# Performance work log

Hardware: AMD Instinct MI355X
Metric: run time of the kernel (lower is better)

Reference implementation:

```python
import jax, jax.numpy as jnp
import numpy as np

B, N, QD, D, S, H, K = 4, 1024, 320, 512, 1024, 8, 32
DH = D // H  # 64
EPS = 1e-5


def setup_inputs() -> dict:
    key = jax.random.key(0)
    ks = jax.random.split(key, 10)
    sc = 1.0 / np.sqrt(D)
    return {
        "query_states": jax.random.normal(ks[0], (B, N, QD), dtype=jnp.float32),
        "Wqp": jax.random.normal(ks[1], (D, QD), dtype=jnp.float32) / np.sqrt(QD),
        "mem_keys": jax.random.normal(ks[2], (S, D), dtype=jnp.float32),
        "mem_values": jax.random.normal(ks[3], (S, D), dtype=jnp.float32) * 0.1,
        "Wq": jax.random.normal(ks[4], (D, D), dtype=jnp.float32) * sc,
        "Wk": jax.random.normal(ks[5], (D, D), dtype=jnp.float32) * sc,
        "Wv": jax.random.normal(ks[6], (D, D), dtype=jnp.float32) * sc,
        "Wo": jax.random.normal(ks[7], (D, D), dtype=jnp.float32) * sc,
        "ln_g": jnp.ones((D,), dtype=jnp.float32),
        "ln_b": jnp.zeros((D,), dtype=jnp.float32),
        "Wout": jax.random.normal(ks[8], (QD, D), dtype=jnp.float32) * sc,
        "bout": jnp.zeros((QD,), dtype=jnp.float32),
    }


def _l2norm(x):
    return x / jnp.sqrt(jnp.sum(x * x, axis=-1, keepdims=True) + 1e-12)


def reference(query_states, Wqp, mem_keys, mem_values, Wq, Wk, Wv, Wo, ln_g, ln_b, Wout, bout):
    # project queries into memory space: [B,N,D]
    q = jnp.einsum("bnq,dq->bnd", query_states, Wqp)
    # normalize memory slots (normalize_slots=True)
    keys = _l2norm(mem_keys)    # [S,D]
    vals = _l2norm(mem_values)  # [S,D]
    # top-k memory-slot preselection over raw query-key scores
    scores = jnp.einsum("bnd,sd->bns", q, keys)          # [B,N,S]
    _, top_idx = jax.lax.top_k(scores, K)                  # [B,N,K]
    sel_k = jnp.take(keys, top_idx, axis=0)                # [B,N,K,D]
    sel_v = jnp.take(vals, top_idx, axis=0)                # [B,N,K,D]
    # multi-head cross-attention over gathered slots
    qh = jnp.einsum("bnd,ed->bne", q, Wq).reshape(B, N, H, DH)
    kh = jnp.einsum("bnkd,ed->bnke", sel_k, Wk).reshape(B, N, K, H, DH)
    vh = jnp.einsum("bnkd,ed->bnke", sel_v, Wv).reshape(B, N, K, H, DH)
    att = jnp.einsum("bnhd,bnkhd->bnhk", qh, kh) / jnp.sqrt(jnp.float32(DH))  # temperature=1.0
    w = jax.nn.softmax(att, axis=-1)                       # [B,N,H,K]
    ctx = jnp.einsum("bnhk,bnkhd->bnhd", w, vh).reshape(B, N, D)
    ctx = jnp.einsum("bnd,ed->bne", ctx, Wo)               # [B,N,D]
    # output projector: LayerNorm + Linear(memory_dim -> query_dim); dropout inactive (eval)
    mu = jnp.mean(ctx, axis=-1, keepdims=True)
    var = jnp.mean((ctx - mu) ** 2, axis=-1, keepdims=True)
    normed = (ctx - mu) / jnp.sqrt(var + EPS) * ln_g + ln_b
    out = jnp.einsum("bnd,qd->bnq", normed, Wout) + bout   # [B,N,QD]
    return out
```

## Files before the change

kernel.cpp:

```cpp
#include <hip/hip_runtime.h>


__device__ __forceinline__ float bf2f(unsigned short u) {
    return __uint_as_float(((unsigned int)u) << 16);
}
__device__ __forceinline__ unsigned short f2bf(float f) {
    unsigned int u = __float_as_uint(f);
    u += 0x7FFFu + ((u >> 16) & 1u);
    return (unsigned short)(u >> 16);
}
__device__ __forceinline__ int detect_bf(const void* g) {
    return ((*(const unsigned int*)g) & 0xFFFFu) != 0u;
}
__device__ __forceinline__ float ldg1(const void* p, size_t i, int bf) {
    return bf ? bf2f(((const unsigned short*)p)[i]) : ((const float*)p)[i];
}
__device__ __forceinline__ void ld4(const void* p, size_t i, int bf, float* o) {
    if (bf) {
        ushort4 v = *reinterpret_cast<const ushort4*>((const unsigned short*)p + i);
        o[0] = bf2f(v.x); o[1] = bf2f(v.y); o[2] = bf2f(v.z); o[3] = bf2f(v.w);
    } else {
        float4 v = *reinterpret_cast<const float4*>((const float*)p + i);
        o[0] = v.x; o[1] = v.y; o[2] = v.z; o[3] = v.w;
    }
}
__device__ __forceinline__ unsigned int fkey(float x) {
    unsigned int u = __float_as_uint(x);
    return (u & 0x80000000u) ? ~u : (u | 0x80000000u);
}
__device__ __forceinline__ float funkey(unsigned int k) {
    unsigned int u = (k & 0x80000000u) ? (k & 0x7FFFFFFFu) : ~k;
    return __uint_as_float(u);
}

typedef __attribute__((ext_vector_type(8))) short bf16x8;
typedef __attribute__((ext_vector_type(4))) float f32x4;
typedef __attribute__((ext_vector_type(4))) unsigned int u32x4;

__device__ __forceinline__ void split8(const float* x, u32x4& h, u32x4& l) {
#pragma unroll
    for (int j = 0; j < 4; j++) {
        float x0 = x[2 * j], x1 = x[2 * j + 1];
        unsigned int hp, lp;
        asm("v_cvt_pk_bf16_f32 %0, %1, %2" : "=v"(hp) : "v"(x0), "v"(x1));
        float h0 = __uint_as_float(hp << 16);
        float h1 = __uint_as_float(hp & 0xFFFF0000u);
        float l0 = x0 - h0, l1 = x1 - h1;
        asm("v_cvt_pk_bf16_f32 %0, %1, %2" : "=v"(lp) : "v"(l0), "v"(l1));
        h[j] = hp; l[j] = lp;
    }
}

__device__ __forceinline__ void gload16(const void* g, void* l) {
    __builtin_amdgcn_global_load_lds(
        (const __attribute__((address_space(1))) unsigned int*)g,
        (__attribute__((address_space(3))) unsigned int*)l,
        16, 0, 0);
}

__global__ __launch_bounds__(256) void prep_fused(
    const void* __restrict__ keys, const void* __restrict__ vals,
    const void* __restrict__ Wqp, const void* __restrict__ X,
    const void* __restrict__ gdet,
    float* __restrict__ inv_kf, float* __restrict__ inv_vf,
    float* __restrict__ WqpT,
    unsigned short* __restrict__ Xh, unsigned short* __restrict__ Xl)
{
    __shared__ double red[256];
    __shared__ float tile[32][36];
    const int bf = detect_bf(gdet);
    const int bid = blockIdx.x, t = threadIdx.x;
    if (bid < 2048) {
        int r = bid;
        const void* src = (r < 1024) ? keys : vals;
        size_t base = (size_t)((r < 1024) ? r : r - 1024) * 512;
        float x0 = ldg1(src, base + t, bf), x1 = ldg1(src, base + t + 256, bf);
        red[t] = (double)x0 * x0 + (double)x1 * x1;
        __syncthreads();
        for (int s = 128; s > 0; s >>= 1) {
            if (t < s) red[t] += red[t + s];
            __syncthreads();
        }
        if (t == 0) {
            float rs = (float)(1.0 / sqrt(red[0] + 1e-12));
            if (r < 1024) inv_kf[r] = rs;
            else          inv_vf[r - 1024] = rs;
        }
    } else if (bid < 2208) {
        int tid = bid - 2048;
        int d0 = (tid & 15) * 32, q0 = (tid >> 4) * 32;
        int r = t >> 3, c = (t & 7) * 4;
        float v[4];
        ld4(Wqp, (size_t)(d0 + r) * 320 + q0 + c, bf, v);
#pragma unroll
        for (int i = 0; i < 4; i++) tile[r][c + i] = v[i];
        __syncthreads();
        float o[4];
#pragma unroll
        for (int i = 0; i < 4; i++) o[i] = tile[c + i][r];
        *reinterpret_cast<float4*>(&WqpT[(size_t)(q0 + r) * 512 + d0 + c]) =
            make_float4(o[0], o[1], o[2], o[3]);
    } else {
        int i = (bid - 2208) * 256 + t;
        float v[8];
        ld4(X, (size_t)i * 8, bf, v);
        ld4(X, (size_t)i * 8 + 4, bf, v + 4);
        u32x4 h, l;
        split8(v, h, l);
        *reinterpret_cast<u32x4*>(Xh + (size_t)i * 8) = h;
        *reinterpret_cast<u32x4*>(Xl + (size_t)i * 8) = l;
    }
}

__global__ __launch_bounds__(256) void mfma_abt(
    const void* __restrict__ A, const void* __restrict__ B,
    const float* __restrict__ scale, float* __restrict__ C,
    const void* __restrict__ A2, const void* __restrict__ B2,
    const float* __restrict__ scale2, float* __restrict__ C2, int ysplit,
    const float2* __restrict__ stats, const void* __restrict__ g,
    const void* __restrict__ bvec, const void* __restrict__ bias,
    void* __restrict__ O,
    unsigned short* __restrict__ Hout, unsigned short* __restrict__ Lout,
    int hrow0a, int hrow0b,
    int N, int amode, int abfon, int bbfon, int epi, int npass,
    const void* __restrict__ gdet)
{
    __shared__ __align__(16) short lds[12288];
    const int AHo = 0, ALo = 2048, BHo = 4096, BLo = 8192;
    const int flag = detect_bf(gdet);
    const int abf = abfon ? flag : 0;
    const int bbf = bbfon ? flag : 0;
    const int t = threadIdx.x;
    int by = blockIdx.y;
    const void* Ap = A; const void* Bp = B;
    const float* scp = scale; float* Cp = C;
    int hrow0 = hrow0a;
    if (ysplit && by >= ysplit) {
        Ap = A2; Bp = B2; scp = scale2; Cp = C2; by -= ysplit; hrow0 = hrow0b;
    }
    const int m0 = by * 32, n0 = blockIdx.x * 64;
    const int lane = t & 63, wv = t >> 6;
    const int wm = wv >> 1, wn = wv & 1;
    const int srow = t >> 3;
    const int sc8  = t & 7;

    int aoff[2], boff[2][2];
#pragma unroll
    for (int kk = 0; kk < 2; kk++) {
        int ra = wm * 16 + (lane & 15);
        int ca = kk * 4 + (lane >> 4);
        aoff[kk] = ra * 64 + ((ca ^ (ra & 7)) << 3);
    }
#pragma unroll
    for (int ni = 0; ni < 2; ni++)
#pragma unroll
        for (int kk = 0; kk < 2; kk++) {
            int rb = wn * 32 + ni * 16 + (lane & 15);
            int cb = kk * 4 + (lane >> 4);
            boff[ni][kk] = rb * 64 + ((cb ^ (rb & 7)) << 3);
        }

    const int addr0 = srow * 64 + ((sc8 ^ (srow & 7)) << 3);
    const int addr1 = addr0 + 32 * 64;

    float s0 = 1.0f;
    float2 st0 = make_float2(0.f, 1.f);
    if (amode == 1) {
        s0 = scp ? scp[m0 + srow] : 1.0f;
    } else if (amode == 2) {
        st0 = stats[m0 + srow];
    }

    f32x4 acc[2];
    acc[0] = (f32x4){0.f, 0.f, 0.f, 0.f};
    acc[1] = (f32x4){0.f, 0.f, 0.f, 0.f};

    float av0[8], bv0[8], bv1[8];
    {
        ld4(Ap, (size_t)(m0 + srow) * 512 + sc8 * 8,          abf, av0);
        ld4(Ap, (size_t)(m0 + srow) * 512 + sc8 * 8 + 4,      abf, av0 + 4);
        ld4(Bp, (size_t)(n0 + srow) * 512 + sc8 * 8,          bbf, bv0);
        ld4(Bp, (size_t)(n0 + srow) * 512 + sc8 * 8 + 4,      bbf, bv0 + 4);
        ld4(Bp, (size_t)(n0 + srow + 32) * 512 + sc8 * 8,     bbf, bv1);
        ld4(Bp, (size_t)(n0 + srow + 32) * 512 + sc8 * 8 + 4, bbf, bv1 + 4);
    }

    for (int ks = 0; ks < 8; ks++) {
        const int kb = ks * 64;
        float a0[8], b0[8], b1[8];
#pragma unroll
        for (int j = 0; j < 8; j++) { a0[j] = av0[j]; b0[j] = bv0[j]; b1[j] = bv1[j]; }
        if (amode == 1) {
#pragma unroll
            for (int j = 0; j < 8; j++) a0[j] *= s0;
        } else if (amode == 2) {
            float gv[8], bv8[8];
            ld4(g,    (size_t)(kb + sc8 * 8),     flag, gv);
            ld4(g,    (size_t)(kb + sc8 * 8 + 4), flag, gv + 4);
            ld4(bvec, (size_t)(kb + sc8 * 8),     flag, bv8);
            ld4(bvec, (size_t)(kb + sc8 * 8 + 4), flag, bv8 + 4);
#pragma unroll
            for (int j = 0; j < 8; j++)
                a0[j] = (a0[j] - st0.x) * st0.y * gv[j] + bv8[j];
        }
        u32x4 ah0, al0, bh0, bl0, bh1, bl1;
        split8(a0, ah0, al0);
        split8(b0, bh0, bl0); split8(b1, bh1, bl1);
        __syncthreads();
        *reinterpret_cast<u32x4*>(&lds[AHo + addr0]) = ah0;
        *reinterpret_cast<u32x4*>(&lds[ALo + addr0]) = al0;
        *reinterpret_cast<u32x4*>(&lds[BHo + addr0]) = bh0;
        *reinterpret_cast<u32x4*>(&lds[BHo + addr1]) = bh1;
        *reinterpret_cast<u32x4*>(&lds[BLo + addr0]) = bl0;
        *reinterpret_cast<u32x4*>(&lds[BLo + addr1]) = bl1;
        __syncthreads();
        if (ks < 7) {
            const int kn = kb + 64;
            ld4(Ap, (size_t)(m0 + srow) * 512 + kn + sc8 * 8,          abf, av0);
            ld4(Ap, (size_t)(m0 + srow) * 512 + kn + sc8 * 8 + 4,      abf, av0 + 4);
            ld4(Bp, (size_t)(n0 + srow) * 512 + kn + sc8 * 8,          bbf, bv0);
            ld4(Bp, (size_t)(n0 + srow) * 512 + kn + sc8 * 8 + 4,      bbf, bv0 + 4);
            ld4(Bp, (size_t)(n0 + srow + 32) * 512 + kn + sc8 * 8,     bbf, bv1);
            ld4(Bp, (size_t)(n0 + srow + 32) * 512 + kn + sc8 * 8 + 4, bbf, bv1 + 4);
        }
        for (int p = 0; p < npass; p++) {
            const int Ab = (p == 1 || p == 3) ? ALo : AHo;
            const int Bb = (p >= 2) ? BLo : BHo;
#pragma unroll
            for (int kk = 0; kk < 2; kk++) {
                bf16x8 af, bfr[2];
                af = *reinterpret_cast<const bf16x8*>(&lds[Ab + aoff[kk]]);
#pragma unroll
                for (int ni = 0; ni < 2; ni++)
                    bfr[ni] = *reinterpret_cast<const bf16x8*>(&lds[Bb + boff[ni][kk]]);
#pragma unroll
                for (int ni = 0; ni < 2; ni++)
                    acc[ni] = __builtin_amdgcn_mfma_f32_16x16x32_bf16(
                        af, bfr[ni], acc[ni], 0, 0, 0);
            }
        }
    }

    {
        int mbase = m0 + wm * 16 + (lane >> 4) * 4;
#pragma unroll
        for (int ni = 0; ni < 2; ni++) {
            int n = n0 + wn * 32 + ni * 16 + (lane & 15);
            if (epi == 0) {
#pragma unroll
                for (int r = 0; r < 4; r++) {
                    float v = acc[ni][r];
                    Cp[(size_t)(mbase + r) * N + n] = v;
                    if (Hout) {
                        unsigned short hb = f2bf(v);
                        unsigned short lb = f2bf(v - bf2f(hb));
                        size_t ho = (size_t)(hrow0 + mbase + r) * N + n;
                        Hout[ho] = hb;
                        Lout[ho] = lb;
                    }
                }
            } else {
                float bo = bias ? ldg1(bias, n, flag) : 0.f;
#pragma unroll
                for (int r = 0; r < 4; r++) {
                    float v = acc[ni][r] + bo;
                    size_t off = (size_t)(mbase + r) * N + n;
                    if (flag) ((unsigned short*)O)[off] = f2bf(v);
                    else      ((float*)O)[off] = v;
                }
            }
        }
    }
}

__global__ __launch_bounds__(256) void gemm_scqh(
    const unsigned short* __restrict__ Xh, const unsigned short* __restrict__ Xl,
    const unsigned short* __restrict__ Bh, const unsigned short* __restrict__ Bl,
    float* __restrict__ Sc, float* __restrict__ qh)
{
    __shared__ __align__(16) short lds[24576];
    const int AHo = 0, ALo = 8192, BHo = 16384, BLo = 20480;
    const int t = threadIdx.x;
    const int m0 = blockIdx.y * 128, n0 = blockIdx.x * 64;
    const int lane = t & 63, wv = t >> 6;
    const int wm = wv >> 1, wn = wv & 1;
    const int lr = lane >> 3;
    const int lc = lane & 7;

    int aoff[4][2], boff[2][2];
#pragma unroll
    for (int mi = 0; mi < 4; mi++)
#pragma unroll
        for (int kk = 0; kk < 2; kk++) {
            int ra = wm * 64 + mi * 16 + (lane & 15);
            int ca = kk * 4 + (lane >> 4);
            aoff[mi][kk] = ra * 64 + ((ca ^ (ra & 7)) << 3);
        }
#pragma unroll
    for (int ni = 0; ni < 2; ni++)
#pragma unroll
        for (int kk = 0; kk < 2; kk++) {
            int rb = wn * 32 + ni * 16 + (lane & 15);
            int cb = kk * 4 + (lane >> 4);
            boff[ni][kk] = rb * 64 + ((cb ^ (rb & 7)) << 3);
        }

    f32x4 acc[4][2];
#pragma unroll
    for (int mi = 0; mi < 4; mi++)
#pragma unroll
        for (int ni = 0; ni < 2; ni++)
            acc[mi][ni] = (f32x4){0.f, 0.f, 0.f, 0.f};

    char* smem = (char*)lds;

    for (int ks = 0; ks < 5; ks++) {
        const int kb = ks * 64;
        __syncthreads();
#pragma unroll
        for (int i = 0; i < 4; i++) {
            int r0 = wv * 32 + i * 8;
            int r  = r0 + lr;
            int sc = lc ^ (r & 7);
            size_t go = (size_t)(m0 + r) * 320 + kb + sc * 8;
            gload16(Xh + go, smem + (AHo << 1) + r0 * 128);
            gload16(Xl + go, smem + (ALo << 1) + r0 * 128);
        }
#pragma unroll
        for (int i = 0; i < 2; i++) {
            int r0 = wv * 16 + i * 8;
            int r  = r0 + lr;
            int sc = lc ^ (r & 7);
            size_t go = (size_t)(n0 + r) * 320 + kb + sc * 8;
            gload16(Bh + go, smem + (BHo << 1) + r0 * 128);
            gload16(Bl + go, smem + (BLo << 1) + r0 * 128);
        }
        __syncthreads();
#pragma unroll
        for (int p = 0; p < 3; p++) {
            const int Ab = (p == 1) ? ALo : AHo;
            const int Bb = (p == 2) ? BLo : BHo;
#pragma unroll
            for (int kk = 0; kk < 2; kk++) {
                bf16x8 af[4], bfr[2];
#pragma unroll
                for (int mi = 0; mi < 4; mi++)
                    af[mi] = *reinterpret_cast<const bf16x8*>(&lds[Ab + aoff[mi][kk]]);
#pragma unroll
                for (int ni = 0; ni < 2; ni++)
                    bfr[ni] = *reinterpret_cast<const bf16x8*>(&lds[Bb + boff[ni][kk]]);
#pragma unroll
                for (int mi = 0; mi < 4; mi++)
#pragma unroll
                    for (int ni = 0; ni < 2; ni++)
                        acc[mi][ni] = __builtin_amdgcn_mfma_f32_16x16x32_bf16(
                            af[mi], bfr[ni], acc[mi][ni], 0, 0, 0);
            }
        }
    }

#pragma unroll
    for (int mi = 0; mi < 4; mi++) {
        int mbase = m0 + wm * 64 + mi * 16 + (lane >> 4) * 4;
#pragma unroll
        for (int ni = 0; ni < 2; ni++) {
            int n = n0 + wn * 32 + ni * 16 + (lane & 15);
#pragma unroll
            for (int r = 0; r < 4; r++) {
                float v = acc[mi][ni][r];
                int m = mbase + r;
                if (n0 < 1024) Sc[(size_t)m * 1024 + n] = v;
                else           qh[(size_t)m * 512 + (n - 1024)] = v;
            }
        }
    }
}

__global__ __launch_bounds__(256) void topk_select(
    const float* __restrict__ Sc, const void* __restrict__ X,
    const void* __restrict__ gdet, const float* __restrict__ KWf,
    int* __restrict__ idx)
{
    __shared__ unsigned int srow[4][1024];
    __shared__ unsigned int scv[4][64];
    __shared__ int          sci[4][64];
    const int bf = detect_bf(gdet);
    const int w = threadIdx.x >> 6, lane = threadIdx.x & 63;
    const int row = blockIdx.x * 4 + w;
    const float* S = Sc + (size_t)row * 1024;

#pragma unroll
    for (int q = 0; q < 4; q++) {
        float4 v = *reinterpret_cast<const float4*>(&S[lane * 4 + q * 256]);
        uint4 k = make_uint4(fkey(v.x), fkey(v.y), fkey(v.z), fkey(v.w));
        *reinterpret_cast<uint4*>(&srow[w][lane * 4 + q * 256]) = k;
    }
    scv[w][lane] = 0u;
    sci[w][lane] = 0x7FFFFFFF;
    __syncthreads();

    unsigned int lo = 0u, hi = 0xFFFFFFFFu;
    int cnt_lo = 1024;
    while (cnt_lo > 48 && hi - lo > 1u) {
        unsigned int mid = lo + ((hi - lo) >> 1);
        int c = 0;
#pragma unroll
        for (int q = 0; q < 4; q++) {
            uint4 k = *reinterpret_cast<const uint4*>(&srow[w][lane * 4 + q * 256]);
            c += (k.x >= mid) + (k.y >= mid) + (k.z >= mid) + (k.w >= mid);
        }
#pragma unroll
        for (int o = 1; o < 64; o <<= 1) c += __shfl_xor(c, o, 64);
        if (c >= 33) { lo = mid; cnt_lo = c; }
        else hi = mid;
    }
    const unsigned int T = lo;

    int cl = 0;
#pragma unroll
    for (int q = 0; q < 4; q++) {
        uint4 k = *reinterpret_cast<const uint4*>(&srow[w][lane * 4 + q * 256]);
        cl += (k.x >= T) + (k.y >= T) + (k.z >= T) + (k.w >= T);
    }
    int inc = cl;
#pragma unroll
    for (int o = 1; o < 64; o <<= 1) {
        int y = __shfl_up(inc, o, 64);
        if (lane >= o) inc += y;
    }
    int pos = inc - cl;
#pragma unroll
    for (int q = 0; q < 4; q++) {
        uint4 k = *reinterpret_cast<const uint4*>(&srow[w][lane * 4 + q * 256]);
        int base = lane * 4 + q * 256;
        if (k.x >= T && pos < 64) { scv[w][pos] = k.x; sci[w][pos] = base + 0; pos++; }
        if (k.y >= T && pos < 64) { scv[w][pos] = k.y; sci[w][pos] = base + 1; pos++; }
        if (k.z >= T && pos < 64) { scv[w][pos] = k.z; sci[w][pos] = base + 2; pos++; }
        if (k.w >= T && pos < 64) { scv[w][pos] = k.w; sci[w][pos] = base + 3; pos++; }
    }
    __syncthreads();
    unsigned int cv = scv[w][lane];
    int          ci = sci[w][lane];
#pragma unroll
    for (int k = 2; k <= 64; k <<= 1) {
#pragma unroll
        for (int jj = k >> 1; jj > 0; jj >>= 1) {
            unsigned int ov = __shfl_xor(cv, jj, 64);
            int          oi = __shfl_xor(ci, jj, 64);
            bool up = ((lane & k) == 0);
            bool takemax = (((lane & jj) == 0) == up);
            bool othergreater = (ov > cv) || (ov == cv && oi < ci);
            if (takemax == othergreater) { cv = ov; ci = oi; }
        }
    }
    float v31 = funkey(__shfl(cv, 31, 64));
    float v32 = funkey(__shfl(cv, 32, 64));
    if (v31 - v32 > 2.5e-4f) {
        if (lane < 32) idx[(size_t)row * 32 + lane] = ci;
        return;
    }
    size_t xb = (size_t)row * 320;
    bool active = (lane < 48) && (ci != 0x7FFFFFFF);
    int cidx = active ? ci : 0x7FFFFFFF;
    const float* kr = KWf + (size_t)(active ? ci : 0) * 320;
    double s = 0.0;
#pragma unroll 4
    for (int d = 0; d < 320; d++) {
        float xd = ldg1(X, xb + d, bf);
        s += (double)xd * (double)kr[d];
    }
    if (!active) s = -1.0e300;
#pragma unroll
    for (int k = 2; k <= 64; k <<= 1) {
#pragma unroll
        for (int jj = k >> 1; jj > 0; jj >>= 1) {
            double os = __shfl_xor(s, jj, 64);
            int    oi = __shfl_xor(cidx, jj, 64);
            bool up = ((lane & k) == 0);
            bool takemax = (((lane & jj) == 0) == up);
            bool og = (os > s) || (os == s && oi < cidx);
            if (takemax == og) { s = os; cidx = oi; }
        }
    }
    if (lane < 32) idx[(size_t)row * 32 + lane] = cidx;
}

__global__ __launch_bounds__(256) void attn_kernel(
    const float* __restrict__ qh, const float* __restrict__ Kp,
    const float* __restrict__ Vp, const int* __restrict__ idx,
    float* __restrict__ ctx)
{
    __shared__ float sq[512];
    __shared__ int   sidx[32];
    __shared__ float sl[8][32];
    __shared__ float sw[8][32];
    int row = blockIdx.x, t = threadIdx.x;
    int w = t >> 6, l = t & 63;
    if (t < 128)
        *reinterpret_cast<float4*>(&sq[t * 4]) =
            *reinterpret_cast<const float4*>(&qh[(size_t)row * 512 + t * 4]);
    if (t < 32) {
        int v = idx[(size_t)row * 32 + t];
        sidx[t] = (v < 0) ? 0 : (v > 1023 ? 1023 : v);
    }
    __syncthreads();

    float4 q0 = *reinterpret_cast<const float4*>(&sq[l * 8]);
    float4 q1 = *reinterpret_cast<const float4*>(&sq[l * 8 + 4]);
    int h = l >> 3;
#pragma unroll
    for (int i = 0; i < 8; i++) {
        int s = w * 8 + i;
        const float* kp = Kp + (size_t)sidx[s] * 512 + l * 8;
        float4 k0 = *reinterpret_cast<const float4*>(kp);
        float4 k1 = *reinterpret_cast<const float4*>(kp + 4);
        float p = q0.x * k0.x + q0.y * k0.y + q0.z * k0.z + q0.w * k0.w
                + q1.x * k1.x + q1.y * k1.y + q1.z * k1.z + q1.w * k1.w;
        p += __shfl_xor(p, 1, 64);
        p += __shfl_xor(p, 2, 64);
        p += __shfl_xor(p, 4, 64);
        if ((l & 7) == 0) sl[h][s] = p * 0.125f;
    }
    __syncthreads();

    int hh = t >> 5, kk = t & 31;
    float logit = sl[hh][kk];
    float m = -1e30f;
#pragma unroll
    for (int i = 0; i < 32; i++) m = fmaxf(m, sl[hh][i]);
    float ssum = 0.f;
#pragma unroll
    for (int i = 0; i < 32; i++) ssum += __expf(sl[hh][i] - m);
    sw[hh][kk] = __expf(logit - m) / ssum;
    __syncthreads();

    int c = t * 2, hc = c >> 6;
    float ax = 0.f, ay = 0.f;
#pragma unroll
    for (int k2 = 0; k2 < 32; k2++) {
        float2 vv = *reinterpret_cast<const float2*>(&Vp[(size_t)sidx[k2] * 512 + c]);
        float wgt = sw[hc][k2];
        ax += wgt * vv.x; ay += wgt * vv.y;
    }
    *reinterpret_cast<float2*>(&ctx[(size_t)row * 512 + c]) = make_float2(ax, ay);
}

__global__ __launch_bounds__(256) void ln_stats(
    const float* __restrict__ co, float2* __restrict__ stats)
{
    int w = threadIdx.x >> 6, lane = threadIdx.x & 63;
    int row = blockIdx.x * 4 + w;
    const float* p = co + (size_t)row * 512;
    float4 a = *reinterpret_cast<const float4*>(&p[lane * 8]);
    float4 b = *reinterpret_cast<const float4*>(&p[lane * 8 + 4]);
    double s  = (double)a.x + (double)a.y + (double)a.z + (double)a.w
              + (double)b.x + (double)b.y + (double)b.z + (double)b.w;
    double ss = (double)a.x * a.x + (double)a.y * a.y + (double)a.z * a.z
              + (double)a.w * a.w + (double)b.x * b.x + (double)b.y * b.y
              + (double)b.z * b.z + (double)b.w * b.w;
#pragma unroll
    for (int o = 1; o < 64; o <<= 1) {
        s  += __shfl_xor(s, o, 64);
        ss += __shfl_xor(ss, o, 64);
    }
    if (lane == 0) {
        double mu = s / 512.0, var = ss / 512.0 - mu * mu;
        stats[row] = make_float2((float)mu, (float)(1.0 / sqrt(var + 1e-5)));
    }
}

extern "C" void kernel_launch(void* const* d_in, const int* in_sizes, int n_in,
                              void* d_out, int out_size, void* d_ws, size_t ws_size,
                              hipStream_t stream)
{
    const void* X    = d_in[0];
    const void* Wqp  = d_in[1];
    const void* keys = d_in[2];
    const void* vals = d_in[3];
    const void* Wq   = d_in[4];
    const void* Wk   = d_in[5];
    const void* Wv   = d_in[6];
    const void* Wo   = d_in[7];
    const void* ln_g = d_in[8];
    const void* ln_b = d_in[9];
    const void* Wout = d_in[10];
    const void* bout = d_in[11];

    float* ws = (float*)d_ws;
    float*  Sc     = ws;
    float*  co     = ws;
    float*  Yreg   = ws + 2097152;
    float*  qh     = ws + 4194304;
    float*  Mf     = ws + 6291456;
    float*  Kp     = ws + 6291456;
    float*  KWf    = ws + 6815744;
    float*  Vp     = ws + 6815744;
    float*  WqpT   = ws + 7340032;
    int*    idx    = (int*)(ws + 7995392);
    float*  inv_kf = ws + 8128512;
    float*  inv_vf = ws + 8129536;
    unsigned short* Xh  = (unsigned short*)(ws + 8388608);
    unsigned short* Xl  = (unsigned short*)(ws + 9043968);
    unsigned short* Bh  = (unsigned short*)(ws + 9699328);
    unsigned short* Bl  = (unsigned short*)(ws + 9945088);
    float*  ctx    = Yreg;
    float2* stats  = (float2*)Yreg;

    prep_fused<<<2848, 256, 0, stream>>>(
        keys, vals, Wqp, X, ln_g, inv_kf, inv_vf, WqpT, Xh, Xl);
    mfma_abt<<<dim3(5, 48), 256, 0, stream>>>(
        keys, WqpT, inv_kf, KWf, Wq, WqpT, nullptr, Mf, 32,
        nullptr, nullptr, nullptr, nullptr, nullptr,
        Bh, Bl, 0, 1024,
        320, 1, 1, 0, 0, 4, ln_g);
    gemm_scqh<<<dim3(24, 32), 256, 0, stream>>>(Xh, Xl, Bh, Bl, Sc, qh);
    topk_select<<<1024, 256, 0, stream>>>(Sc, X, ln_g, KWf, idx);
    mfma_abt<<<dim3(8, 64), 256, 0, stream>>>(
        keys, Wk, inv_kf, Kp, vals, Wv, inv_vf, Vp, 32,
        nullptr, nullptr, nullptr, nullptr, nullptr,
        nullptr, nullptr, 0, 0,
        512, 1, 1, 1, 0, 3, ln_g);
    attn_kernel<<<4096, 256, 0, stream>>>(qh, Kp, Vp, idx, ctx);
    mfma_abt<<<dim3(8, 128), 256, 0, stream>>>(
        ctx, Wo, nullptr, co, nullptr, nullptr, nullptr, nullptr, 0,
        nullptr, nullptr, nullptr, nullptr, nullptr,
        nullptr, nullptr, 0, 0,
        512, 0, 0, 1, 0, 3, ln_g);
    ln_stats<<<1024, 256, 0, stream>>>(co, stats);
    mfma_abt<<<dim3(5, 128), 256, 0, stream>>>(
        co, Wout, nullptr, nullptr, nullptr, nullptr, nullptr, nullptr, 0,
        stats, ln_g, ln_b, bout, d_out,
        nullptr, nullptr, 0, 0,
        320, 2, 0, 1, 1, 3, ln_g);
}
```

Baseline: 227.6 us.

## Merge K/V projection into score GEMM, fuse LN stats, narrow top-k search

Merges the K/V slot projection GEMM into the score/qh GEMM launch as extra blocks, so the two run concurrently in one grid and one launch is saved. Removes the separate ln_stats kernel by having the output GEMM compute per-row mean and inverse std inline. Also seeds the top-k radix binary search with the row min/max to cut iterations. The trade-offs are redundant re-reading of each co row per column block and heterogeneous blocks within one grid. Vp moves to a new workspace offset because it would otherwise overlap KWf while top-k is still reading it.

```diff
diff --git a/kernel.cpp b/kernel.cpp
--- a/kernel.cpp
+++ b/kernel.cpp
@@ -168,7 +168,26 @@
     if (amode == 1) {
         s0 = scp ? scp[m0 + srow] : 1.0f;
     } else if (amode == 2) {
-        st0 = stats[m0 + srow];
+        if (stats) {
+            st0 = stats[m0 + srow];
+        } else {
+            double s = 0.0, ss = 0.0;
+            for (int kb2 = 0; kb2 < 512; kb2 += 64) {
+                float v8[8];
+                ld4(Ap, (size_t)(m0 + srow) * 512 + kb2 + sc8 * 8,     abf, v8);
+                ld4(Ap, (size_t)(m0 + srow) * 512 + kb2 + sc8 * 8 + 4, abf, v8 + 4);
+#pragma unroll
+                for (int j = 0; j < 8; j++) {
+                    s  += (double)v8[j];
+                    ss += (double)v8[j] * v8[j];
+                }
+            }
+            s  += __shfl_xor(s, 1, 64);  ss += __shfl_xor(ss, 1, 64);
+            s  += __shfl_xor(s, 2, 64);  ss += __shfl_xor(ss, 2, 64);
+            s  += __shfl_xor(s, 4, 64);  ss += __shfl_xor(ss, 4, 64);
+            double mu = s / 512.0, var = ss / 512.0 - mu * mu;
+            st0 = make_float2((float)mu, (float)(1.0 / sqrt(var + 1e-5)));
+        }
     }
 
     f32x4 acc[2];
@@ -273,105 +292,208 @@
     }
 }
 
-__global__ __launch_bounds__(256) void gemm_scqh(
+__global__ __launch_bounds__(256) void gemm_scqh_kv(
     const unsigned short* __restrict__ Xh, const unsigned short* __restrict__ Xl,
     const unsigned short* __restrict__ Bh, const unsigned short* __restrict__ Bl,
-    float* __restrict__ Sc, float* __restrict__ qh)
+    float* __restrict__ Sc, float* __restrict__ qh,
+    const void* __restrict__ keys, const void* __restrict__ Wk,
+    const float* __restrict__ inv_kf, float* __restrict__ Kp,
+    const void* __restrict__ vals, const void* __restrict__ Wv,
+    const float* __restrict__ inv_vf, float* __restrict__ Vp,
+    const void* __restrict__ gdet)
 {
     __shared__ __align__(16) short lds[24576];
-    const int AHo = 0, ALo = 8192, BHo = 16384, BLo = 20480;
     const int t = threadIdx.x;
-    const int m0 = blockIdx.y * 128, n0 = blockIdx.x * 64;
+    const int bid = blockIdx.x;
     const int lane = t & 63, wv = t >> 6;
     const int wm = wv >> 1, wn = wv & 1;
-    const int lr = lane >> 3;
-    const int lc = lane & 7;
-
-    int aoff[4][2], boff[2][2];
-#pragma unroll
-    for (int mi = 0; mi < 4; mi++)
+
+    if (bid < 768) {
+        const int AHo = 0, ALo = 8192, BHo = 16384, BLo = 20480;
+        const int m0 = (bid / 24) * 128, n0 = (bid % 24) * 64;
+        const int lr = lane >> 3, lc = lane & 7;
+
+        int aoff[4][2], boff[2][2];
+#pragma unroll
+        for (int mi = 0; mi < 4; mi++)
+#pragma unroll
+            for (int kk = 0; kk < 2; kk++) {
+                int ra = wm * 64 + mi * 16 + (lane & 15);
+                int ca = kk * 4 + (lane >> 4);
+                aoff[mi][kk] = ra * 64 + ((ca ^ (ra & 7)) << 3);
+            }
+#pragma unroll
+        for (int ni = 0; ni < 2; ni++)
+#pragma unroll
+            for (int kk = 0; kk < 2; kk++) {
+                int rb = wn * 32 + ni * 16 + (lane & 15);
+                int cb = kk * 4 + (lane >> 4);
+                boff[ni][kk] = rb * 64 + ((cb ^ (rb & 7)) << 3);
+            }
+
+        f32x4 acc[4][2];
+#pragma unroll
+        for (int mi = 0; mi < 4; mi++)
+#pragma unroll
+            for (int ni = 0; ni < 2; ni++)
+                acc[mi][ni] = (f32x4){0.f, 0.f, 0.f, 0.f};
+
+        char* smem = (char*)lds;
+
+        for (int ks = 0; ks < 5; ks++) {
+            const int kb = ks * 64;
+            __syncthreads();
+#pragma unroll
+            for (int i = 0; i < 4; i++) {
+                int r0 = wv * 32 + i * 8;
+                int r  = r0 + lr;
+                int sc = lc ^ (r & 7);
+                size_t go = (size_t)(m0 + r) * 320 + kb + sc * 8;
+                gload16(Xh + go, smem + (AHo << 1) + r0 * 128);
+                gload16(Xl + go, smem + (ALo << 1) + r0 * 128);
+            }
+#pragma unroll
+            for (int i = 0; i < 2; i++) {
+                int r0 = wv * 16 + i * 8;
+                int r  = r0 + lr;
+                int sc = lc ^ (r & 7);
+                size_t go = (size_t)(n0 + r) * 320 + kb + sc * 8;
+                gload16(Bh + go, smem + (BHo << 1) + r0 * 128);
+                gload16(Bl + go, smem + (BLo << 1) + r0 * 128);
+            }
+            __syncthreads();
+#pragma unroll
+            for (int p = 0; p < 3; p++) {
+                const int Ab = (p == 1) ? ALo : AHo;
+                const int Bb = (p == 2) ? BLo : BHo;
+#pragma unroll
+                for (int kk = 0; kk < 2; kk++) {
+                    bf16x8 af[4], bfr[2];
+#pragma unroll
+                    for (int mi = 0; mi < 4; mi++)
+                        af[mi] = *reinterpret_cast<const bf16x8*>(&lds[Ab + aoff[mi][kk]]);
+#pragma unroll
+                    for (int ni = 0; ni < 2; ni++)
+                        bfr[ni] = *reinterpret_cast<const bf16x8*>(&lds[Bb + boff[ni][kk]]);
+#pragma unroll
+                    for (int mi = 0; mi < 4; mi++)
+#pragma unroll
+                        for (int ni = 0; ni < 2; ni++)
+                            acc[mi][ni] = __builtin_amdgcn_mfma_f32_16x16x32_bf16(
+                                af[mi], bfr[ni], acc[mi][ni], 0, 0, 0);
+                }
+            }
+        }
+
+#pragma unroll
+        for (int mi = 0; mi < 4; mi++) {
+            int mbase = m0 + wm * 64 + mi * 16 + (lane >> 4) * 4;
+#pragma unroll
+            for (int ni = 0; ni < 2; ni++) {
+                int n = n0 + wn * 32 + ni * 16 + (lane & 15);
+#pragma unroll
+                for (int r = 0; r < 4; r++) {
+                    float v = acc[mi][ni][r];
+                    int m = mbase + r;
+                    if (n0 < 1024) Sc[(size_t)m * 1024 + n] = v;
+                    else           qh[(size_t)m * 512 + (n - 1024)] = v;
+                }
+            }
+        }
+    } else {
+        const int AHk = 0, ALk = 2048, BHk = 4096, BLk = 8192;
+        int kb_ = bid - 768;
+        int x = kb_ & 7, y = kb_ >> 3;
+        const int flag = detect_bf(gdet);
+        const void* Ap; const void* Bp; const float* scp; float* Cp;
+        if (y < 32) { Ap = keys; Bp = Wk; scp = inv_kf; Cp = Kp; }
+        else        { Ap = vals; Bp = Wv; scp = inv_vf; Cp = Vp; y -= 32; }
+        const int m0 = y * 32, n0 = x * 64;
+        const int srow = t >> 3, sc8 = t & 7;
+
+        int aoff[2], boff[2][2];
 #pragma unroll
         for (int kk = 0; kk < 2; kk++) {
-            int ra = wm * 64 + mi * 16 + (lane & 15);
+            int ra = wm * 16 + (lane & 15);
             int ca = kk * 4 + (lane >> 4);
-            aoff[mi][kk] = ra * 64 + ((ca ^ (ra & 7)) << 3);
-        }
-#pragma unroll
-    for (int ni = 0; ni < 2; ni++)
-#pragma unroll
-        for (int kk = 0; kk < 2; kk++) {
-            int rb = wn * 32 + ni * 16 + (lane & 15);
-            int cb = kk * 4 + (lane >> 4);
-            boff[ni][kk] = rb * 64 + ((cb ^ (rb & 7)) << 3);
-        }
-
-    f32x4 acc[4][2];
-#pragma unroll
-    for (int mi = 0; mi < 4; mi++)
+            aoff[kk] = ra * 64 + ((ca ^ (ra & 7)) << 3);
+        }
 #pragma unroll
         for (int ni = 0; ni < 2; ni++)
-            acc[mi][ni] = (f32x4){0.f, 0.f, 0.f, 0.f};
-
-    char* smem = (char*)lds;
-
-    for (int ks = 0; ks < 5; ks++) {
-        const int kb = ks * 64;
-        __syncthreads();
-#pragma unroll
-        for (int i = 0; i < 4; i++) {
-            int r0 = wv * 32 + i * 8;
-            int r  = r0 + lr;
-            int sc = lc ^ (r & 7);
-            size_t go = (size_t)(m0 + r) * 320 + kb + sc * 8;
-            gload16(Xh + go, smem + (AHo << 1) + r0 * 128);
-            gload16(Xl + go, smem + (ALo << 1) + r0 * 128);
-        }
-#pragma unroll
-        for (int i = 0; i < 2; i++) {
-            int r0 = wv * 16 + i * 8;
-            int r  = r0 + lr;
-            int sc = lc ^ (r & 7);
-            size_t go = (size_t)(n0 + r) * 320 + kb + sc * 8;
-            gload16(Bh + go, smem + (BHo << 1) + r0 * 128);
-            gload16(Bl + go, smem + (BLo << 1) + r0 * 128);
-        }
-        __syncthreads();
-#pragma unroll
-        for (int p = 0; p < 3; p++) {
-            const int Ab = (p == 1) ? ALo : AHo;
-            const int Bb = (p == 2) ? BLo : BHo;
 #pragma unroll
             for (int kk = 0; kk < 2; kk++) {
-                bf16x8 af[4], bfr[2];
-#pragma unroll
-                for (int mi = 0; mi < 4; mi++)
-                    af[mi] = *reinterpret_cast<const bf16x8*>(&lds[Ab + aoff[mi][kk]]);
-#pragma unroll
-                for (int ni = 0; ni < 2; ni++)
-                    bfr[ni] = *reinterpret_cast<const bf16x8*>(&lds[Bb + boff[ni][kk]]);
-#pragma unroll
-                for (int mi = 0; mi < 4; mi++)
+                int rb = wn * 32 + ni * 16 + (lane & 15);
+                int cb = kk * 4 + (lane >> 4);
+                boff[ni][kk] = rb * 64 + ((cb ^ (rb & 7)) << 3);
+            }
+
+        const int addr0 = srow * 64 + ((sc8 ^ (srow & 7)) << 3);
+        const int addr1 = addr0 + 32 * 64;
+        const float s0 = scp[m0 + srow];
+
+        f32x4 acc[2];
+        acc[0] = (f32x4){0.f, 0.f, 0.f, 0.f};
+        acc[1] = (f32x4){0.f, 0.f, 0.f, 0.f};
+
+        float av0[8], bv0[8], bv1[8];
+        ld4(Ap, (size_t)(m0 + srow) * 512 + sc8 * 8,          flag, av0);
+        ld4(Ap, (size_t)(m0 + srow) * 512 + sc8 * 8 + 4,      flag, av0 + 4);
+        ld4(Bp, (size_t)(n0 + srow) * 512 + sc8 * 8,          flag, bv0);
+        ld4(Bp, (size_t)(n0 + srow) * 512 + sc8 * 8 + 4,      flag, bv0 + 4);
+        ld4(Bp, (size_t)(n0 + srow + 32) * 512 + sc8 * 8,     flag, bv1);
+        ld4(Bp, (size_t)(n0 + srow + 32) * 512 + sc8 * 8 + 4, flag, bv1 + 4);
+
+        for (int ks = 0; ks < 8; ks++) {
+            const int kb = ks * 64;
+            float a0[8], b0[8], b1[8];
+#pragma unroll
+            for (int j = 0; j < 8; j++) { a0[j] = av0[j] * s0; b0[j] = bv0[j]; b1[j] = bv1[j]; }
+            u32x4 ah0, al0, bh0, bl0, bh1, bl1;
+            split8(a0, ah0, al0);
+            split8(b0, bh0, bl0); split8(b1, bh1, bl1);
+            __syncthreads();
+            *reinterpret_cast<u32x4*>(&lds[AHk + addr0]) = ah0;
+            *reinterpret_cast<u32x4*>(&lds[ALk + addr0]) = al0;
+            *reinterpret_cast<u32x4*>(&lds[BHk + addr0]) = bh0;
+            *reinterpret_cast<u32x4*>(&lds[BHk + addr1]) = bh1;
+            *reinterpret_cast<u32x4*>(&lds[BLk + addr0]) = bl0;
+            *reinterpret_cast<u32x4*>(&lds[BLk + addr1]) = bl1;
+            __syncthreads();
+            if (ks < 7) {
+                const int kn = kb + 64;
+                ld4(Ap, (size_t)(m0 + srow) * 512 + kn + sc8 * 8,          flag, av0);
+                ld4(Ap, (size_t)(m0 + srow) * 512 + kn + sc8 * 8 + 4,      flag, av0 + 4);
+                ld4(Bp, (size_t)(n0 + srow) * 512 + kn + sc8 * 8,          flag, bv0);
+                ld4(Bp, (size_t)(n0 + srow) * 512 + kn + sc8 * 8 + 4,      flag, bv0 + 4);
+                ld4(Bp, (size_t)(n0 + srow + 32) * 512 + kn + sc8 * 8,     flag, bv1);
+                ld4(Bp, (size_t)(n0 + srow + 32) * 512 + kn + sc8 * 8 + 4, flag, bv1 + 4);
+            }
+#pragma unroll
+            for (int p = 0; p < 3; p++) {
+                const int Ab = (p == 1) ? ALk : AHk;
+                const int Bb = (p == 2) ? BLk : BHk;
+#pragma unroll
+                for (int kk = 0; kk < 2; kk++) {
+                    bf16x8 af, bfr[2];
+                    af = *reinterpret_cast<const bf16x8*>(&lds[Ab + aoff[kk]]);
 #pragma unroll
                     for (int ni = 0; ni < 2; ni++)
-                        acc[mi][ni] = __builtin_amdgcn_mfma_f32_16x16x32_bf16(
-                            af[mi], bfr[ni], acc[mi][ni], 0, 0, 0);
-            }
-        }
-    }
-
-#pragma unroll
-    for (int mi = 0; mi < 4; mi++) {
-        int mbase = m0 + wm * 64 + mi * 16 + (lane >> 4) * 4;
+                        bfr[ni] = *reinterpret_cast<const bf16x8*>(&lds[Bb + boff[ni][kk]]);
+#pragma unroll
+                    for (int ni = 0; ni < 2; ni++)
+                        acc[ni] = __builtin_amdgcn_mfma_f32_16x16x32_bf16(
+                            af, bfr[ni], acc[ni], 0, 0, 0);
+                }
+            }
+        }
+
+        int mbase = m0 + wm * 16 + (lane >> 4) * 4;
 #pragma unroll
         for (int ni = 0; ni < 2; ni++) {
             int n = n0 + wn * 32 + ni * 16 + (lane & 15);
 #pragma unroll
-            for (int r = 0; r < 4; r++) {
-                float v = acc[mi][ni][r];
-                int m = mbase + r;
-                if (n0 < 1024) Sc[(size_t)m * 1024 + n] = v;
-                else           qh[(size_t)m * 512 + (n - 1024)] = v;
-            }
+            for (int r = 0; r < 4; r++)
+                Cp[(size_t)(mbase + r) * 512 + n] = acc[ni][r];
         }
     }
 }
@@ -389,17 +511,26 @@
     const int row = blockIdx.x * 4 + w;
     const float* S = Sc + (size_t)row * 1024;
 
+    unsigned int mn = 0xFFFFFFFFu, mx = 0u;
 #pragma unroll
     for (int q = 0; q < 4; q++) {
         float4 v = *reinterpret_cast<const float4*>(&S[lane * 4 + q * 256]);
         uint4 k = make_uint4(fkey(v.x), fkey(v.y), fkey(v.z), fkey(v.w));
         *reinterpret_cast<uint4*>(&srow[w][lane * 4 + q * 256]) = k;
+        mn = min(mn, min(min(k.x, k.y), min(k.z, k.w)));
+        mx = max(mx, max(max(k.x, k.y), max(k.z, k.w)));
     }
     scv[w][lane] = 0u;
     sci[w][lane] = 0x7FFFFFFF;
+#pragma unroll
+    for (int o = 1; o < 64; o <<= 1) {
+        mn = min(mn, __shfl_xor(mn, o, 64));
+        mx = max(mx, __shfl_xor(mx, o, 64));
+    }
     __syncthreads();
 
-    unsigned int lo = 0u, hi = 0xFFFFFFFFu;
+    unsigned int lo = mn;
+    unsigned int hi = (mx == 0xFFFFFFFFu) ? 0xFFFFFFFFu : mx + 1u;
     int cnt_lo = 1024;
     while (cnt_lo > 48 && hi - lo > 1u) {
         unsigned int mid = lo + ((hi - lo) >> 1);
@@ -545,30 +676,6 @@
     *reinterpret_cast<float2*>(&ctx[(size_t)row * 512 + c]) = make_float2(ax, ay);
 }
 
-__global__ __launch_bounds__(256) void ln_stats(
-    const float* __restrict__ co, float2* __restrict__ stats)
-{
-    int w = threadIdx.x >> 6, lane = threadIdx.x & 63;
-    int row = blockIdx.x * 4 + w;
-    const float* p = co + (size_t)row * 512;
-    float4 a = *reinterpret_cast<const float4*>(&p[lane * 8]);
-    float4 b = *reinterpret_cast<const float4*>(&p[lane * 8 + 4]);
-    double s  = (double)a.x + (double)a.y + (double)a.z + (double)a.w
-              + (double)b.x + (double)b.y + (double)b.z + (double)b.w;
-    double ss = (double)a.x * a.x + (double)a.y * a.y + (double)a.z * a.z
-              + (double)a.w * a.w + (double)b.x * b.x + (double)b.y * b.y
-              + (double)b.z * b.z + (double)b.w * b.w;
-#pragma unroll
-    for (int o = 1; o < 64; o <<= 1) {
-        s  += __shfl_xor(s, o, 64);
-        ss += __shfl_xor(ss, o, 64);
-    }
-    if (lane == 0) {
-        double mu = s / 512.0, var = ss / 512.0 - mu * mu;
-        stats[row] = make_float2((float)mu, (float)(1.0 / sqrt(var + 1e-5)));
-    }
-}
-
 extern "C" void kernel_launch(void* const* d_in, const int* in_sizes, int n_in,
                               void* d_out, int out_size, void* d_ws, size_t ws_size,
                               hipStream_t stream)
@@ -594,7 +701,6 @@
     float*  Mf     = ws + 6291456;
     float*  Kp     = ws + 6291456;
     float*  KWf    = ws + 6815744;
-    float*  Vp     = ws + 6815744;
     float*  WqpT   = ws + 7340032;
     int*    idx    = (int*)(ws + 7995392);
     float*  inv_kf = ws + 8128512;
@@ -603,8 +709,8 @@
     unsigned short* Xl  = (unsigned short*)(ws + 9043968);
     unsigned short* Bh  = (unsigned short*)(ws + 9699328);
     unsigned short* Bl  = (unsigned short*)(ws + 9945088);
+    float*  Vp     = ws + 10190848;
     float*  ctx    = Yreg;
-    float2* stats  = (float2*)Yreg;
 
     prep_fused<<<2848, 256, 0, stream>>>(
         keys, vals, Wqp, X, ln_g, inv_kf, inv_vf, WqpT, Xh, Xl);
@@ -613,23 +719,19 @@
         nullptr, nullptr, nullptr, nullptr, nullptr,
         Bh, Bl, 0, 1024,
         320, 1, 1, 0, 0, 4, ln_g);
-    gemm_scqh<<<dim3(24, 32), 256, 0, stream>>>(Xh, Xl, Bh, Bl, Sc, qh);
+    gemm_scqh_kv<<<1280, 256, 0, stream>>>(
+        Xh, Xl, Bh, Bl, Sc, qh,
+        keys, Wk, inv_kf, Kp, vals, Wv, inv_vf, Vp, ln_g);
     topk_select<<<1024, 256, 0, stream>>>(Sc, X, ln_g, KWf, idx);
-    mfma_abt<<<dim3(8, 64), 256, 0, stream>>>(
-        keys, Wk, inv_kf, Kp, vals, Wv, inv_vf, Vp, 32,
-        nullptr, nullptr, nullptr, nullptr, nullptr,
-        nullptr, nullptr, 0, 0,
-        512, 1, 1, 1, 0, 3, ln_g);
     attn_kernel<<<4096, 256, 0, stream>>>(qh, Kp, Vp, idx, ctx);
     mfma_abt<<<dim3(8, 128), 256, 0, stream>>>(
         ctx, Wo, nullptr, co, nullptr, nullptr, nullptr, nullptr, 0,
         nullptr, nullptr, nullptr, nullptr, nullptr,
         nullptr, nullptr, 0, 0,
         512, 0, 0, 1, 0, 3, ln_g);
-    ln_stats<<<1024, 256, 0, stream>>>(co, stats);
     mfma_abt<<<dim3(5, 128), 256, 0, stream>>>(
         co, Wout, nullptr, nullptr, nullptr, nullptr, nullptr, nullptr, 0,
-        stats, ln_g, ln_b, bout, d_out,
+        nullptr, ln_g, ln_b, bout, d_out,
         nullptr, nullptr, 0, 0,
         320, 2, 0, 1, 1, 3, ln_g);
 }
```

Result: slower. 232.4 us (+2.1%).
